# Kernel optimization log

Measured on AMD Instinct MI355X. Metric: run time of the kernel, lower is better.

Reference implementation:

```python
import jax, jax.numpy as jnp
import numpy as np

N_NODES = 50000
N_EDGES = 800000
D_IN = 128
D_OUT = 128
BN_EPS = 1e-5

# (component index, sign) per (column block j, row block i) of the octonion
# Hamilton matrix, matching make_octonion_mul's cat order exactly.
_OCT_TABLE = [
    [(0, 1), (1, -1), (2, -1), (3, -1), (4, -1), (5, -1), (6, -1), (7, -1)],
    [(1, 1), (0, 1), (3, -1), (2, 1), (5, -1), (4, 1), (7, 1), (6, -1)],
    [(2, 1), (3, 1), (0, 1), (1, -1), (6, -1), (7, -1), (4, 1), (5, 1)],
    [(3, 1), (2, -1), (1, 1), (0, 1), (7, -1), (6, 1), (5, -1), (4, 1)],
    [(4, 1), (5, 1), (6, 1), (7, 1), (0, 1), (1, -1), (2, -1), (3, -1)],
    [(5, 1), (4, -1), (7, 1), (6, -1), (1, 1), (0, 1), (3, 1), (2, -1)],
    [(6, 1), (7, -1), (4, -1), (5, 1), (2, 1), (3, -1), (0, 1), (1, 1)],
    [(7, 1), (6, 1), (5, -1), (4, -1), (3, 1), (2, 1), (1, -1), (0, 1)],
]


def make_octonion_mul(kernel):
    # kernel: [D_IN//8, D_OUT] -> hamilton: [D_IN, D_OUT]
    e = jnp.split(kernel, 8, axis=1)
    cols = [jnp.concatenate([s * e[i] for (i, s) in col], axis=0)
            for col in _OCT_TABLE]
    return jnp.concatenate(cols, axis=1)


def setup_inputs() -> dict:
    key = jax.random.key(0)
    k1, k2, k3, k4, k5 = jax.random.split(key, 5)
    stdv = np.sqrt(6.0 / (D_IN // 8 + D_OUT))
    return {
        "input": jax.random.normal(k1, (N_NODES, D_IN), dtype=jnp.float32),
        "adj_row": jax.random.randint(k2, (N_EDGES,), 0, N_NODES, dtype=jnp.int32),
        "adj_col": jax.random.randint(k3, (N_EDGES,), 0, N_NODES, dtype=jnp.int32),
        "adj_val": jax.random.uniform(k4, (N_EDGES,), dtype=jnp.float32),
        "weight": jax.random.uniform(k5, (D_IN // 8, D_OUT), dtype=jnp.float32,
                                     minval=-stdv, maxval=stdv),
        "gamma": jnp.ones((D_OUT,), dtype=jnp.float32),
        "beta": jnp.zeros((D_OUT,), dtype=jnp.float32),
    }


def reference(input, adj_row, adj_col, adj_val, weight, gamma, beta):
    hamilton = make_octonion_mul(weight)             # [D_IN, D_OUT]
    support = input @ hamilton                       # [N, D_OUT]
    # sparse adjacency spmm: out[r] += val * support[c]
    msg = adj_val[:, None] * support[adj_col]        # [E, D_OUT]
    out = jax.ops.segment_sum(msg, adj_row, num_segments=N_NODES)
    # BatchNorm1d (training mode: biased batch stats), then tanh
    mean = jnp.mean(out, axis=0)
    var = jnp.var(out, axis=0)
    normed = (out - mean) / jnp.sqrt(var + BN_EPS) * gamma + beta
    return jnp.tanh(normed)
```

## Files before the change

kernel.cpp:

```cpp
#include <hip/hip_runtime.h>
#include <hip/hip_fp16.h>
#include <math.h>

#define N_NODES 50000
#define N_EDGES 800000
#define D 128
#define BN_EPS 1e-5f
#define N_TILES 3125
#define CAP 48
#define SPMM_BLOCKS 2048
#define SCOLS 32
#define BINS 512
#define RPB 98
#define EPB 3125
#define SORTB 256
#define BCAP 2048
#define GEMMB 782

typedef __attribute__((ext_vector_type(8))) _Float16 half8;
typedef __attribute__((ext_vector_type(4))) float floatx4;

__device__ __constant__ int OCT_C[8][8] = {
    {0,1,2,3,4,5,6,7},
    {1,0,3,2,5,4,7,6},
    {2,3,0,1,6,7,4,5},
    {3,2,1,0,7,6,5,4},
    {4,5,6,7,0,1,2,3},
    {5,4,7,6,1,0,3,2},
    {6,7,4,5,2,3,0,1},
    {7,6,5,4,3,2,1,0}};
__device__ __constant__ float OCT_S[8][8] = {
    { 1,-1,-1,-1,-1,-1,-1,-1},
    { 1, 1,-1, 1,-1, 1, 1,-1},
    { 1, 1, 1,-1,-1,-1, 1, 1},
    { 1,-1, 1, 1,-1, 1,-1, 1},
    { 1, 1, 1, 1, 1,-1,-1,-1},
    { 1,-1, 1,-1, 1, 1, 1,-1},
    { 1,-1,-1, 1, 1,-1, 1, 1},
    { 1, 1,-1,-1, 1, 1,-1, 1}};

__global__ __launch_bounds__(256) void setup_kernel(const float* __restrict__ W,
                                                    __half* __restrict__ Ht,
                                                    float* __restrict__ stats,
                                                    int* __restrict__ bintail) {
    const int i = blockIdx.x * 256 + threadIdx.x;
    if (i < D * D) {
        int ccol = i >> 7, k = i & 127;
        int ii = k >> 4, kw = k & 15, j = ccol >> 4, m = ccol & 15;
        Ht[i] = __float2half(OCT_S[j][ii] * W[kw * D + OCT_C[j][ii] * 16 + m]);
    }
    if (i < 2 * D) stats[i] = 0.0f;
    if (i < BINS * 16) bintail[i] = 0;
}

__global__ __launch_bounds__(256) void sortgemm_kernel(const int* __restrict__ arow,
                                                       const int* __restrict__ acol,
                                                       const float* __restrict__ aval,
                                                       int* __restrict__ bintail,
                                                       uint2* __restrict__ binned,
                                                       const float* __restrict__ in,
                                                       const __half* __restrict__ Ht,
                                                       __half* __restrict__ support) {
    __shared__ int hist[BINS], lbase[BINS], hist2[BINS];
    const int b = blockIdx.x;
    const int tid = threadIdx.x;
    if (b < SORTB) {
        for (int k = tid; k < BINS; k += 256) hist[k] = 0;
        __syncthreads();
        const int e0 = b * EPB, e1 = e0 + EPB;
        for (int i = e0 + tid; i < e1; i += 256) {
            int bin = arow[i] / RPB;
            atomicAdd(&hist[bin], 1);
        }
        __syncthreads();
        for (int k = tid; k < BINS; k += 256) {
            lbase[k] = atomicAdd(&bintail[k * 16], hist[k]);
            hist2[k] = 0;
        }
        __syncthreads();
        for (int i = e0 + tid; i < e1; i += 256) {
            int r = arow[i];
            int bin = r / RPB;
            unsigned hv = (unsigned)__half_as_ushort(__float2half(aval[i]));
            unsigned pk = ((unsigned)acol[i] & 0xFFFFu) | (hv << 16);
            int k = atomicAdd(&hist2[bin], 1);
            int idx = lbase[bin] + k;
            if (idx < BCAP) binned[(size_t)bin * BCAP + idx] = make_uint2(pk, (unsigned)r);
        }
        return;
    }
    const int wv = tid >> 6;
    const int tile = (b - SORTB) * 4 + wv;
    if (tile >= N_TILES) return;
    const int lane = tid & 63;
    const int s = lane & 15;
    const int t = lane >> 4;

    half8 bb[8][4];
#pragma unroll
    for (int kk = 0; kk < 4; ++kk)
#pragma unroll
        for (int n = 0; n < 8; ++n)
            bb[n][kk] = *reinterpret_cast<const half8*>(Ht + (size_t)(16 * n + s) * D + kk * 32 + 8 * t);

    const float* ap = in + (size_t)(tile * 16 + s) * D;
    half8 a[4];
#pragma unroll
    for (int kk = 0; kk < 4; ++kk) {
        float4 f0 = *reinterpret_cast<const float4*>(ap + kk * 32 + 8 * t);
        float4 f1 = *reinterpret_cast<const float4*>(ap + kk * 32 + 8 * t + 4);
        a[kk][0] = (_Float16)f0.x; a[kk][1] = (_Float16)f0.y;
        a[kk][2] = (_Float16)f0.z; a[kk][3] = (_Float16)f0.w;
        a[kk][4] = (_Float16)f1.x; a[kk][5] = (_Float16)f1.y;
        a[kk][6] = (_Float16)f1.z; a[kk][7] = (_Float16)f1.w;
    }

    floatx4 acc[8];
#pragma unroll
    for (int n = 0; n < 8; ++n) acc[n] = (floatx4){0.f, 0.f, 0.f, 0.f};
#pragma unroll
    for (int kk = 0; kk < 4; ++kk)
#pragma unroll
        for (int n = 0; n < 8; ++n)
            acc[n] = __builtin_amdgcn_mfma_f32_16x16x32_f16(a[kk], bb[n][kk], acc[n], 0, 0, 0);

    __half* sp = support + (size_t)(tile * 16 + 4 * t) * D + s;
#pragma unroll
    for (int r = 0; r < 4; ++r)
#pragma unroll
        for (int n = 0; n < 8; ++n)
            sp[(size_t)r * D + 16 * n] = __float2half(acc[n][r]);
}

__global__ __launch_bounds__(256) void spmm_kernel(const int* __restrict__ bintail,
                                                   const uint2* __restrict__ binned,
                                                   const __half* __restrict__ support,
                                                   __half* __restrict__ outh,
                                                   float* __restrict__ colsum,
                                                   float* __restrict__ colsq) {
    __shared__ unsigned lbucket[RPB * CAP];
    __shared__ int lcnt[RPB];
    __shared__ float lsum[SCOLS], lsq[SCOLS];

    const int tid = threadIdx.x;
    const int b = blockIdx.x;
    const int slice = (b & 7) >> 1;
    const int rank = ((b >> 3) << 1) | (b & 1);
    const int rbase = rank * RPB;

    if (tid < RPB) lcnt[tid] = 0;
    if (tid < SCOLS) { lsum[tid] = 0.f; lsq[tid] = 0.f; }
    for (int k = tid; k < RPB * CAP; k += 256) lbucket[k] = 0u;
    __syncthreads();
    int nb = bintail[rank * 16];
    nb = nb < BCAP ? nb : BCAP;
    const unsigned long long* seg = reinterpret_cast<const unsigned long long*>(
        binned + (size_t)rank * BCAP);
    for (int i = tid; i < nb; i += 256) {
        unsigned long long e = __builtin_nontemporal_load(seg + i);
        int rl = (int)(e >> 32) - rbase;
        int slot = atomicAdd(&lcnt[rl], 1);
        if (slot < CAP) lbucket[rl * CAP + slot] = (unsigned)e;
    }
    __syncthreads();

    const int lane = tid & 63;
    const int wv = tid >> 6;
    const int h = lane >> 4;
    const int cl = lane & 15;
    const int colbase = slice * SCOLS + cl * 2;
    const unsigned cb2 = (unsigned)(colbase * 2);
    const char* sbase = reinterpret_cast<const char*>(support);

    float s0 = 0.f, s1 = 0.f, q0 = 0.f, q1 = 0.f;

    for (int rl = wv * 2; rl < RPB; rl += 8) {
        const int row = rbase + rl;
        const int rowb = row + 1;
        int na = lcnt[rl]; na = na < CAP ? na : CAP;
        int nb2 = (rl + 1 < RPB) ? lcnt[rl + 1] : 0; nb2 = nb2 < CAP ? nb2 : CAP;
        const int nmax = na > nb2 ? na : nb2;
        __half2 acca = __half2half2(__ushort_as_half((unsigned short)0));
        __half2 accb = acca;

        {
            unsigned ua[8], ub[8];
            __half2 ga[8], gb[8];
#pragma unroll
            for (int j = 0; j < 8; ++j) {
                ua[j] = lbucket[rl * CAP + j * 4 + h];
                ub[j] = lbucket[(rl + 1 < RPB ? rl + 1 : rl) * CAP + j * 4 + h];
            }
            if (rl + 1 >= RPB) {
#pragma unroll
                for (int j = 0; j < 8; ++j) ub[j] = 0u;
            }
#pragma unroll
            for (int j = 0; j < 8; ++j) {
                ga[j] = *reinterpret_cast<const __half2*>(sbase + (((ua[j] & 0xFFFFu) << 8) + cb2));
                gb[j] = *reinterpret_cast<const __half2*>(sbase + (((ub[j] & 0xFFFFu) << 8) + cb2));
            }
#pragma unroll
            for (int j = 0; j < 8; ++j) {
                unsigned va2 = __builtin_amdgcn_perm(ua[j], ua[j], 0x07060706u);
                unsigned vb2 = __builtin_amdgcn_perm(ub[j], ub[j], 0x07060706u);
                acca = __hfma2(*reinterpret_cast<__half2*>(&va2), ga[j], acca);
                accb = __hfma2(*reinterpret_cast<__half2*>(&vb2), gb[j], accb);
            }
        }
        if (nmax > 32) {
            unsigned ua[4], ub[4];
            __half2 ga[4], gb[4];
#pragma unroll
            for (int j = 0; j < 4; ++j) {
                ua[j] = lbucket[rl * CAP + 32 + j * 4 + h];
                ub[j] = lbucket[(rl + 1 < RPB ? rl + 1 : rl) * CAP + 32 + j * 4 + h];
            }
            if (rl + 1 >= RPB) {
#pragma unroll
                for (int j = 0; j < 4; ++j) ub[j] = 0u;
            }
#pragma unroll
            for (int j = 0; j < 4; ++j) {
                ga[j] = *reinterpret_cast<const __half2*>(sbase + (((ua[j] & 0xFFFFu) << 8) + cb2));
                gb[j] = *reinterpret_cast<const __half2*>(sbase + (((ub[j] & 0xFFFFu) << 8) + cb2));
            }
#pragma unroll
            for (int j = 0; j < 4; ++j) {
                unsigned va2 = __builtin_amdgcn_perm(ua[j], ua[j], 0x07060706u);
                unsigned vb2 = __builtin_amdgcn_perm(ub[j], ub[j], 0x07060706u);
                acca = __hfma2(*reinterpret_cast<__half2*>(&va2), ga[j], acca);
                accb = __hfma2(*reinterpret_cast<__half2*>(&vb2), gb[j], accb);
            }
        }

#pragma unroll
        for (int off = 16; off <= 32; off <<= 1) {
            int ia = __shfl_xor(*reinterpret_cast<int*>(&acca), off);
            int ib = __shfl_xor(*reinterpret_cast<int*>(&accb), off);
            acca = __hadd2(acca, *reinterpret_cast<__half2*>(&ia));
            accb = __hadd2(accb, *reinterpret_cast<__half2*>(&ib));
        }
        if (h == 0) {
            if (row < N_NODES) {
                float2 fa = __half22float2(acca);
                __builtin_nontemporal_store(*reinterpret_cast<unsigned*>(&acca),
                    reinterpret_cast<unsigned*>(outh + (size_t)row * D + colbase));
                s0 += fa.x; s1 += fa.y; q0 += fa.x * fa.x; q1 += fa.y * fa.y;
            }
            if (rowb < N_NODES && rl + 1 < RPB) {
                float2 fb = __half22float2(accb);
                __builtin_nontemporal_store(*reinterpret_cast<unsigned*>(&accb),
                    reinterpret_cast<unsigned*>(outh + (size_t)rowb * D + colbase));
                s0 += fb.x; s1 += fb.y; q0 += fb.x * fb.x; q1 += fb.y * fb.y;
            }
        }
    }

    if (h == 0) {
        atomicAdd(&lsum[cl * 2 + 0], s0); atomicAdd(&lsum[cl * 2 + 1], s1);
        atomicAdd(&lsq[cl * 2 + 0], q0);  atomicAdd(&lsq[cl * 2 + 1], q1);
    }
    __syncthreads();
    if (tid < SCOLS) {
        atomicAdd(&colsum[slice * SCOLS + tid], lsum[tid]);
        atomicAdd(&colsq[slice * SCOLS + tid], lsq[tid]);
    }
}

__global__ __launch_bounds__(256) void bn_tanh_kernel(const __half* __restrict__ outh,
                                                      float* __restrict__ out,
                                                      const float* __restrict__ colsum,
                                                      const float* __restrict__ colsq,
                                                      const float* __restrict__ gamma,
                                                      const float* __restrict__ beta) {
    __shared__ float scale[D], shift[D];
    const int tid = threadIdx.x;
    if (tid < D) {
        float mean = colsum[tid] * (1.0f / N_NODES);
        float var  = colsq[tid] * (1.0f / N_NODES) - mean * mean;
        float sc   = rsqrtf(var + BN_EPS) * gamma[tid];
        scale[tid] = sc;
        shift[tid] = beta[tid] - mean * sc;
    }
    __syncthreads();
    const int nq = N_NODES * D / 8;
    floatx4* outv = reinterpret_cast<floatx4*>(out);
    for (int i = blockIdx.x * 256 + tid; i < nq; i += gridDim.x * 256) {
        uint4 v = reinterpret_cast<const uint4*>(outh)[i];
        const int c = (i & 15) * 8;
        float r[8];
        float2 f;
        f = __half22float2(*reinterpret_cast<__half2*>(&v.x)); r[0] = f.x; r[1] = f.y;
        f = __half22float2(*reinterpret_cast<__half2*>(&v.y)); r[2] = f.x; r[3] = f.y;
        f = __half22float2(*reinterpret_cast<__half2*>(&v.z)); r[4] = f.x; r[5] = f.y;
        f = __half22float2(*reinterpret_cast<__half2*>(&v.w)); r[6] = f.x; r[7] = f.y;
#pragma unroll
        for (int k = 0; k < 8; ++k) {
            float x = r[k] * scale[c + k] + shift[c + k];
            float e = __expf(2.0f * x);
            r[k] = 1.0f - 2.0f / (1.0f + e);
        }
        floatx4 o0 = {r[0], r[1], r[2], r[3]};
        floatx4 o1 = {r[4], r[5], r[6], r[7]};
        __builtin_nontemporal_store(o0, outv + i * 2 + 0);
        __builtin_nontemporal_store(o1, outv + i * 2 + 1);
    }
}

extern "C" void kernel_launch(void* const* d_in, const int* in_sizes, int n_in,
                              void* d_out, int out_size, void* d_ws, size_t ws_size,
                              hipStream_t stream) {
    const float* input  = (const float*)d_in[0];
    const int*   arow   = (const int*)d_in[1];
    const int*   acol   = (const int*)d_in[2];
    const float* aval   = (const float*)d_in[3];
    const float* weight = (const float*)d_in[4];
    const float* gamma  = (const float*)d_in[5];
    const float* beta   = (const float*)d_in[6];
    float* out = (float*)d_out;

    __half*   support = (__half*)d_ws;
    __half*   outh    = (__half*)(support + (size_t)N_NODES * D);
    uint2*    binned  = (uint2*)(outh + (size_t)N_NODES * D);
    float*    colsum  = (float*)(binned + (size_t)BINS * BCAP);
    float*    colsq   = colsum + D;
    int*      bintail = (int*)(colsum + 2 * D);
    __half*   Ht      = (__half*)(bintail + BINS * 16);

    setup_kernel<<<64, 256, 0, stream>>>(weight, Ht, colsum, bintail);
    sortgemm_kernel<<<SORTB + GEMMB, 256, 0, stream>>>(arow, acol, aval, bintail, binned,
                                                       input, Ht, support);
    spmm_kernel<<<SPMM_BLOCKS, 256, 0, stream>>>(bintail, binned, support, outh,
                                                 colsum, colsq);
    bn_tanh_kernel<<<2048, 256, 0, stream>>>(outh, out, colsum, colsq, gamma, beta);
}
```

Baseline: 89.25 us.

## Replace single-pass edge binning with two-pass coarse/fine staged radix scatter

The single-pass histogram scatter into 512 bins is replaced with a two-level partition. Sort blocks first stage edges in LDS into 8 coarse groups and flush them in 64-entry chunks. A new pass-B kernel then scatters each coarse group into 64 fine bins, again in coalesced chunks. This targets the scattered, poorly coalesced global writes and per-bin atomics of the original scatter. In exchange it adds an extra kernel launch and another global read/write of all edges, reusing the outh buffer as coarse storage, plus many block-level barriers.

```diff
diff --git a/kernel.cpp b/kernel.cpp
--- a/kernel.cpp
+++ b/kernel.cpp
@@ -16,6 +16,14 @@
 #define SORTB 256
 #define BCAP 2048
 #define GEMMB 782
+#define NCOARSE 8
+#define CAPA 320
+#define CHUNKA 64
+#define CCAP 106496
+#define NFINE 64
+#define CAPB 64
+#define CHUNKB 32
+#define PASSB_BLOCKS 256
 
 typedef __attribute__((ext_vector_type(8))) _Float16 half8;
 typedef __attribute__((ext_vector_type(4))) float floatx4;
@@ -42,7 +50,8 @@
 __global__ __launch_bounds__(256) void setup_kernel(const float* __restrict__ W,
                                                     __half* __restrict__ Ht,
                                                     float* __restrict__ stats,
-                                                    int* __restrict__ bintail) {
+                                                    int* __restrict__ bintail,
+                                                    int* __restrict__ coarsetail) {
     const int i = blockIdx.x * 256 + threadIdx.x;
     if (i < D * D) {
         int ccol = i >> 7, k = i & 127;
@@ -51,41 +60,74 @@
     }
     if (i < 2 * D) stats[i] = 0.0f;
     if (i < BINS * 16) bintail[i] = 0;
+    if (i < NCOARSE * 16) coarsetail[i] = 0;
 }
 
 __global__ __launch_bounds__(256) void sortgemm_kernel(const int* __restrict__ arow,
                                                        const int* __restrict__ acol,
                                                        const float* __restrict__ aval,
-                                                       int* __restrict__ bintail,
-                                                       uint2* __restrict__ binned,
+                                                       int* __restrict__ coarsetail,
+                                                       uint2* __restrict__ coarse,
                                                        const float* __restrict__ in,
                                                        const __half* __restrict__ Ht,
                                                        __half* __restrict__ support) {
-    __shared__ int hist[BINS], lbase[BINS], hist2[BINS];
+    __shared__ uint2 stageA[NCOARSE * CAPA];
+    __shared__ int fillA[NCOARSE], nfA[NCOARSE], fbA[NCOARSE];
     const int b = blockIdx.x;
     const int tid = threadIdx.x;
     if (b < SORTB) {
-        for (int k = tid; k < BINS; k += 256) hist[k] = 0;
+        if (tid < NCOARSE) fillA[tid] = 0;
         __syncthreads();
         const int e0 = b * EPB, e1 = e0 + EPB;
-        for (int i = e0 + tid; i < e1; i += 256) {
-            int bin = arow[i] / RPB;
-            atomicAdd(&hist[bin], 1);
-        }
-        __syncthreads();
-        for (int k = tid; k < BINS; k += 256) {
-            lbase[k] = atomicAdd(&bintail[k * 16], hist[k]);
-            hist2[k] = 0;
-        }
-        __syncthreads();
-        for (int i = e0 + tid; i < e1; i += 256) {
-            int r = arow[i];
-            int bin = r / RPB;
-            unsigned hv = (unsigned)__half_as_ushort(__float2half(aval[i]));
-            unsigned pk = ((unsigned)acol[i] & 0xFFFFu) | (hv << 16);
-            int k = atomicAdd(&hist2[bin], 1);
-            int idx = lbase[bin] + k;
-            if (idx < BCAP) binned[(size_t)bin * BCAP + idx] = make_uint2(pk, (unsigned)r);
+        for (int base = e0; base < e1; base += 256) {
+            const int i = base + tid;
+            if (i < e1) {
+                int r = arow[i];
+                int bin = r / RPB;
+                int g = bin >> 6;
+                unsigned hv = (unsigned)__half_as_ushort(__float2half(aval[i]));
+                unsigned pk = ((unsigned)acol[i] & 0xFFFFu) | (hv << 16);
+                int pos = atomicAdd(&fillA[g], 1);
+                stageA[g * CAPA + pos] = make_uint2(pk, (unsigned)r);
+            }
+            __syncthreads();
+            if (tid < NCOARSE) {
+                int n = fillA[tid];
+                int nf = n & ~(CHUNKA - 1);
+                nfA[tid] = nf;
+                fbA[tid] = nf ? atomicAdd(&coarsetail[tid * 16], nf) : 0;
+            }
+            __syncthreads();
+            for (int g = 0; g < NCOARSE; ++g) {
+                int nf = nfA[g];
+                if (!nf) continue;
+                int wl = CCAP - fbA[g]; if (wl < 0) wl = 0;
+                int nw = nf < wl ? nf : wl;
+                uint2* dst = coarse + (size_t)g * CCAP + fbA[g];
+                for (int j = tid; j < nw; j += 256) dst[j] = stageA[g * CAPA + j];
+            }
+            __syncthreads();
+            for (int g = 0; g < NCOARSE; ++g) {
+                int n = fillA[g], nf = nfA[g];
+                if (tid < n - nf) stageA[g * CAPA + tid] = stageA[g * CAPA + nf + tid];
+            }
+            __syncthreads();
+            if (tid < NCOARSE) fillA[tid] -= nfA[tid];
+            __syncthreads();
+        }
+        if (tid < NCOARSE) {
+            int n = fillA[tid];
+            nfA[tid] = n;
+            fbA[tid] = n ? atomicAdd(&coarsetail[tid * 16], n) : 0;
+        }
+        __syncthreads();
+        for (int g = 0; g < NCOARSE; ++g) {
+            int n = nfA[g];
+            if (!n) continue;
+            int wl = CCAP - fbA[g]; if (wl < 0) wl = 0;
+            int nw = n < wl ? n : wl;
+            uint2* dst = coarse + (size_t)g * CCAP + fbA[g];
+            for (int j = tid; j < nw; j += 256) dst[j] = stageA[g * CAPA + j];
         }
         return;
     }
@@ -130,6 +172,83 @@
 #pragma unroll
         for (int n = 0; n < 8; ++n)
             sp[(size_t)r * D + 16 * n] = __float2half(acc[n][r]);
+}
+
+__global__ __launch_bounds__(256) void passb_kernel(const int* __restrict__ coarsetail,
+                                                    const uint2* __restrict__ coarse,
+                                                    int* __restrict__ bintail,
+                                                    uint2* __restrict__ binned) {
+    __shared__ uint2 stageB[NFINE * CAPB];
+    __shared__ int fillB[NFINE], nfB[NFINE], fbB[NFINE], stB[NFINE];
+    const int b = blockIdx.x;
+    const int tid = threadIdx.x;
+    const int g = b & 7;
+    const int sr = b >> 3;
+    const int finebase = g * NFINE;
+    int ng = coarsetail[g * 16];
+    if (ng > CCAP) ng = CCAP;
+    const int per = (ng + 31) / 32;
+    const int s0 = sr * per;
+    int s1 = s0 + per; if (s1 > ng) s1 = ng;
+    const uint2* src = coarse + (size_t)g * CCAP;
+
+    if (tid < NFINE) fillB[tid] = 0;
+    __syncthreads();
+
+    for (int base = s0; base < s1; base += 256) {
+        const int i = base + tid;
+        if (i < s1) {
+            uint2 e = src[i];
+            int bin = (int)e.y / RPB;
+            int lb = bin & 63;
+            int pos = atomicAdd(&fillB[lb], 1);
+            if (pos < CAPB) {
+                stageB[lb * CAPB + pos] = e;
+            } else {
+                int idx = atomicAdd(&bintail[bin * 16], 1);
+                if (idx < BCAP) binned[(size_t)bin * BCAP + idx] = e;
+            }
+        }
+        __syncthreads();
+        if (tid < NFINE) {
+            int n = fillB[tid]; if (n > CAPB) n = CAPB;
+            stB[tid] = n;
+            int nf = n & ~(CHUNKB - 1);
+            nfB[tid] = nf;
+            fbB[tid] = nf ? atomicAdd(&bintail[(finebase + tid) * 16], nf) : 0;
+        }
+        __syncthreads();
+        for (int fb = 0; fb < NFINE; ++fb) {
+            int nf = nfB[fb];
+            if (!nf) continue;
+            int wl = BCAP - fbB[fb]; if (wl < 0) wl = 0;
+            int nw = nf < wl ? nf : wl;
+            uint2* dst = binned + (size_t)(finebase + fb) * BCAP + fbB[fb];
+            for (int j = tid; j < nw; j += 256) dst[j] = stageB[fb * CAPB + j];
+        }
+        __syncthreads();
+        for (int fb = 0; fb < NFINE; ++fb) {
+            int n = stB[fb], nf = nfB[fb];
+            if (tid < n - nf) stageB[fb * CAPB + tid] = stageB[fb * CAPB + nf + tid];
+        }
+        __syncthreads();
+        if (tid < NFINE) fillB[tid] = stB[tid] - nfB[tid];
+        __syncthreads();
+    }
+    if (tid < NFINE) {
+        int n = fillB[tid];
+        nfB[tid] = n;
+        fbB[tid] = n ? atomicAdd(&bintail[(finebase + tid) * 16], n) : 0;
+    }
+    __syncthreads();
+    for (int fb = 0; fb < NFINE; ++fb) {
+        int n = nfB[fb];
+        if (!n) continue;
+        int wl = BCAP - fbB[fb]; if (wl < 0) wl = 0;
+        int nw = n < wl ? n : wl;
+        uint2* dst = binned + (size_t)(finebase + fb) * BCAP + fbB[fb];
+        for (int j = tid; j < nw; j += 256) dst[j] = stageB[fb * CAPB + j];
+    }
 }
 
 __global__ __launch_bounds__(256) void spmm_kernel(const int* __restrict__ bintail,
@@ -320,17 +439,20 @@
     const float* beta   = (const float*)d_in[6];
     float* out = (float*)d_out;
 
-    __half*   support = (__half*)d_ws;
-    __half*   outh    = (__half*)(support + (size_t)N_NODES * D);
-    uint2*    binned  = (uint2*)(outh + (size_t)N_NODES * D);
-    float*    colsum  = (float*)(binned + (size_t)BINS * BCAP);
-    float*    colsq   = colsum + D;
-    int*      bintail = (int*)(colsum + 2 * D);
-    __half*   Ht      = (__half*)(bintail + BINS * 16);
-
-    setup_kernel<<<64, 256, 0, stream>>>(weight, Ht, colsum, bintail);
-    sortgemm_kernel<<<SORTB + GEMMB, 256, 0, stream>>>(arow, acol, aval, bintail, binned,
+    __half*   support   = (__half*)d_ws;
+    __half*   outh      = (__half*)(support + (size_t)N_NODES * D);
+    uint2*    coarse    = (uint2*)outh;
+    uint2*    binned    = (uint2*)(outh + (size_t)N_NODES * D);
+    float*    colsum    = (float*)(binned + (size_t)BINS * BCAP);
+    float*    colsq     = colsum + D;
+    int*      bintail   = (int*)(colsum + 2 * D);
+    int*      coarsetail= bintail + BINS * 16;
+    __half*   Ht        = (__half*)(coarsetail + NCOARSE * 16);
+
+    setup_kernel<<<64, 256, 0, stream>>>(weight, Ht, colsum, bintail, coarsetail);
+    sortgemm_kernel<<<SORTB + GEMMB, 256, 0, stream>>>(arow, acol, aval, coarsetail, coarse,
                                                        input, Ht, support);
+    passb_kernel<<<PASSB_BLOCKS, 256, 0, stream>>>(coarsetail, coarse, bintail, binned);
     spmm_kernel<<<SPMM_BLOCKS, 256, 0, stream>>>(bintail, binned, support, outh,
                                                  colsum, colsq);
     bn_tanh_kernel<<<2048, 256, 0, stream>>>(outh, out, colsum, colsq, gamma, beta);
```

After: 238.6 us. 2.67x slower.
